# Kernel tuning notes

Measured on AMD Instinct MI355X. Metric: run time of the kernel, lower is better.

Reference implementation:

```python
import jax, jax.numpy as jnp
import numpy as np

EPS = 1e-5

def conv2d(x, w, b=None, pad=1):
    y = jax.lax.conv_general_dilated(x, w, (1, 1), [(pad, pad), (pad, pad)],
                                     dimension_numbers=('NCHW', 'OIHW', 'NCHW'))
    if b is not None:
        y = y + b[None, :, None, None]
    return y

def batchnorm(x, g, b):
    m = x.mean((0, 2, 3), keepdims=True)
    v = x.var((0, 2, 3), keepdims=True)
    return g[None, :, None, None] * (x - m) * jax.lax.rsqrt(v + EPS) + b[None, :, None, None]

def local_conv(x, w12):
    # x: [B,Ci,H,W]; w12: [B,Ci*9,H,W] -> per-pixel depthwise 3x3 conv
    B, Ci, H, W = x.shape
    xp = jnp.pad(x, ((0, 0), (0, 0), (1, 1), (1, 1)))
    patches = jnp.stack([xp[:, :, dh:dh + H, dw:dw + W]
                         for dh in range(3) for dw in range(3)], axis=2)  # [B,Ci,9,H,W]
    return (patches * w12.reshape(B, Ci, 9, H, W)).sum(axis=2)

def setup_inputs() -> dict:
    key = jax.random.key(0)
    ks = jax.random.split(key, 20)
    B, Ci, Cw, H, W = 4, 64, 64, 128, 128
    s = 0.05
    return {
        'input': jax.random.normal(ks[0], (B, Ci, H, W), jnp.float32),
        'weight': jax.random.normal(ks[1], (B, Cw, H, W), jnp.float32),
        'w_conv11': jax.random.normal(ks[2], (Ci, Ci + Cw, 3, 3), jnp.float32) * s,
        'b_conv11': jnp.zeros((Ci,), jnp.float32),
        'w_conv12': jax.random.normal(ks[3], (Ci * 9, Ci, 3, 3), jnp.float32) * s,
        'b_conv12': jnp.zeros((Ci * 9,), jnp.float32),
        'w_conv21': jax.random.normal(ks[4], (Ci, Ci + Cw, 3, 3), jnp.float32) * s,
        'b_conv21': jnp.zeros((Ci,), jnp.float32),
        'w_conv22': jax.random.normal(ks[5], (Ci * Ci, Ci, 1, 1), jnp.float32) * s,
        'b_conv22': jnp.zeros((Ci * Ci,), jnp.float32),
        'local_bn_g': jnp.ones((Ci,), jnp.float32),
        'local_bn_b': jnp.zeros((Ci,), jnp.float32),
        'br_g': jnp.ones((Ci,), jnp.float32),
        'br_b': jnp.zeros((Ci,), jnp.float32),
        'w_conv3': jax.random.normal(ks[6], (Ci, Ci, 3, 3), jnp.float32) * s,
        'conv3_bn_g': jnp.ones((Ci,), jnp.float32),
        'conv3_bn_b': jnp.zeros((Ci,), jnp.float32),
    }

def reference(input, weight, w_conv11, b_conv11, w_conv12, b_conv12,
              w_conv21, b_conv21, w_conv22, b_conv22,
              local_bn_g, local_bn_b, br_g, br_b,
              w_conv3, conv3_bn_g, conv3_bn_b):
    B, Ci, H, W = input.shape
    cat = jnp.concatenate([input, weight], axis=1)
    w11 = jax.nn.relu(conv2d(cat, w_conv11, b_conv11))
    w12 = conv2d(w11, w_conv12, b_conv12)                      # [B,Ci*9,H,W]
    w21 = jax.nn.relu(conv2d(cat, w_conv21, b_conv21))
    pooled = w21.mean((2, 3), keepdims=True)                   # [B,Ci,1,1]
    w22 = conv2d(pooled, w_conv22, b_conv22, pad=0).reshape(B, Ci, Ci)
    out1 = jax.nn.relu(batchnorm(local_conv(input, w12), local_bn_g, local_bn_b))
    out2 = jnp.einsum('bij,bjn->bin', w22, out1.reshape(B, Ci, H * W)).reshape(B, Ci, H, W)
    out3 = jax.nn.relu(batchnorm(out2, br_g, br_b))
    out4 = jax.nn.relu(batchnorm(conv2d(out3, w_conv3, None), conv3_bn_g, conv3_bn_b))
    return out4
```

## Files before the change

kernel.cpp:

```cpp
#include <hip/hip_runtime.h>

#define EPSV 1e-5f
#define HP 130
#define HW 16384

typedef unsigned int u32;
typedef unsigned short bfu;
typedef __bf16 bf16x8 __attribute__((ext_vector_type(8)));
typedef float  f32x4  __attribute__((ext_vector_type(4)));

__device__ __forceinline__ bfu f2bf(float f){
  u32 u = __builtin_bit_cast(u32, f);
  return (bfu)((u + 0x7FFFu + ((u >> 16) & 1u)) >> 16);
}
__device__ __forceinline__ float bf2f(bfu h){
  return __builtin_bit_cast(float, ((u32)h) << 16);
}
__device__ __forceinline__ f32x4 mfma16(bf16x8 a, bf16x8 b, f32x4 c){
  return __builtin_amdgcn_mfma_f32_16x16x32_bf16(a, b, c, 0, 0, 0);
}
__device__ __forceinline__ bf16x8 ldsfrag(const bfu* p){
  return __builtin_bit_cast(bf16x8, *(const uint4*)p);
}
__device__ __forceinline__ void gload_lds16(const uint4* g, uint4* l){
  __builtin_amdgcn_global_load_lds(
      (const __attribute__((address_space(1))) unsigned int*)g,
      (__attribute__((address_space(3))) unsigned int*)l, 16, 0, 0);
}


__global__ void k_zero_border(bfu* catT, bfu* w11T, bfu* out3T){
  int i = blockIdx.x*256 + threadIdx.x;
  if (i >= 4*516) return;
  int b = i/516, r = i - b*516;
  int hp, wpp;
  if (r < 130){ hp = 0; wpp = r; }
  else if (r < 260){ hp = 129; wpp = r - 130; }
  else { int r2 = r - 260; hp = 1 + (r2 >> 1); wpp = (r2 & 1)*129; }
  int pix = (b*HP + hp)*HP + wpp;
  uint4 z = {0,0,0,0};
  uint4* c4 = (uint4*)catT  + (size_t)pix*16;
  uint4* w4 = (uint4*)w11T  + (size_t)pix*8;
  uint4* o4 = (uint4*)out3T + (size_t)pix*8;
  #pragma unroll
  for (int k = 0; k < 16; ++k) c4[k] = z;
  #pragma unroll
  for (int k = 0; k < 8; ++k){ w4[k] = z; o4[k] = z; }
}

__global__ void k_prep_w(const float* __restrict__ w11w, const float* __restrict__ w21w,
                         const float* __restrict__ w12w, const float* __restrict__ w3w,
                         bfu* A11, bfu* A12, bfu* A3){
  const int total = 147456 + 331776 + 36864;
  for (int i = blockIdx.x*256 + threadIdx.x; i < total; i += gridDim.x*256){
    float v; bfu* dst;
    if (i < 147456){
      int tap = i >> 14, och = (i >> 7) & 127, cin = i & 127;
      v = (och < 64) ? w11w[(och*128 + cin)*9 + tap] : w21w[((och-64)*128 + cin)*9 + tap];
      dst = A11 + i;
    } else if (i < 147456 + 331776){
      int i2 = i - 147456;
      int g = i2 >> 12, t = g/9, tap2 = g%9;
      int c = (i2 >> 6) & 63, j = i2 & 63;
      v = w12w[((c*9 + t)*64 + j)*9 + tap2];
      dst = A12 + i2;
    } else {
      int i3 = i - (147456 + 331776);
      int tap2 = i3 >> 12, oc = (i3 >> 6) & 63, j = i3 & 63;
      v = w3w[(oc*64 + j)*9 + tap2];
      dst = A3 + i3;
    }
    *dst = f2bf(v);
  }
}

__global__ void k_prep_cat(const float* __restrict__ inp, const float* __restrict__ wgt, bfu* catT){
  __shared__ bfu lds[128*136];
  int b = blockIdx.y, h = blockIdx.x;
  int t = threadIdx.x;
  int w = t & 127, c0 = t >> 7;
  #pragma unroll 1
  for (int c = c0; c < 128; c += 2){
    const float* src = (c < 64) ? inp + ((b*64 + c)*128 + h)*128
                                : wgt + ((b*64 + (c-64))*128 + h)*128;
    lds[w*136 + c] = f2bf(src[w]);
  }
  __syncthreads();
  uint4* dst = (uint4*)catT;
  #pragma unroll
  for (int k = 0; k < 8; ++k){
    int idx = k*256 + t;
    int pix = idx >> 4, sub = idx & 15;
    uint4 v = *(const uint4*)&lds[pix*136 + sub*8];
    dst[(((b*HP + h+1)*HP) + (pix+1))*16 + sub] = v;
  }
}

__global__ __launch_bounds__(256) void k1_conv(
    const bfu* __restrict__ catT, const bfu* __restrict__ A11,
    const float* __restrict__ b11, const float* __restrict__ b21,
    bfu* __restrict__ w11T, float* __restrict__ poolP){
  __shared__ bfu ldsC[180*128];
  __shared__ bfu ldsA[2*8192];
  __shared__ float statsF[128];
  int tid = threadIdx.x;
  int b = blockIdx.y, tile = blockIdx.x;
  int h0 = (tile >> 3)*8, w0 = (tile & 7)*16;

  int wid = tid >> 6, l = tid & 63, lg = l >> 4, pc = l & 15;
  int wm = wid >> 1, wn = wid & 1;
  int pcT = tid & 15, lgT = (tid >> 4) & 3;

  const uint4* A4 = (const uint4*)A11;
  uint4* ldsA4 = (uint4*)ldsA;

  #pragma unroll
  for (int k = 0; k < 4; ++k){
    int q = k*4 + wid;
    int row = (q >> 1)*16 + pcT;
    gload_lds16(A4 + row*16 + (q&1)*4 + lgT, ldsA4 + k*256 + wid*64);
  }

  const uint4* catT4 = (const uint4*)catT;
  for (int s = tid; s < 180*16; s += 256){
    int cell = s >> 4, sub = s & 15;
    int th = cell/18, tw = cell - th*18;
    uint4 v = catT4[(((b*HP + h0+th)*HP) + (w0+tw))*16 + sub];
    *(uint4*)&ldsC[cell*128 + ((sub*8) ^ ((cell&7)<<3))] = v;
  }
  __syncthreads();

  f32x4 acc[4][4];
  #pragma unroll
  for (int i = 0; i < 4; ++i)
    #pragma unroll
    for (int j = 0; j < 4; ++j) acc[i][j] = f32x4{0.f,0.f,0.f,0.f};

  int cur = 0;
  #pragma unroll 1
  for (int cc = 0; cc < 18; ++cc){
    int tap = cc >> 1, p = cc & 1;
    if (cc < 17){
      int cc1 = cc + 1, tap1 = cc1 >> 1, p1 = cc1 & 1;
      #pragma unroll
      for (int k = 0; k < 4; ++k){
        int q = k*4 + wid;
        int row = (q >> 1)*16 + pcT;
        gload_lds16(A4 + tap1*2048 + row*16 + p1*8 + (q&1)*4 + lgT,
                    ldsA4 + (cur^1)*1024 + k*256 + wid*64);
      }
    }
    int kh = (tap >= 6) ? 2 : ((tap >= 3) ? 1 : 0);
    int kw = tap - kh*3;
    #pragma unroll
    for (int jq = 0; jq < 2; ++jq){
      int jc = p*2 + jq;
      bf16x8 a[4], bb[4];
      #pragma unroll
      for (int fm = 0; fm < 4; ++fm)
        a[fm] = __builtin_bit_cast(bf16x8, ldsA4[cur*1024 + ((wm*4 + fm)*2 + jq)*64 + l]);
      #pragma unroll
      for (int fn = 0; fn < 4; ++fn){
        int cell = (wn*4 + fn + kh)*18 + (pc + kw);
        bb[fn] = ldsfrag(&ldsC[cell*128 + ((jc*32 + lg*8) ^ ((cell&7)<<3))]);
      }
      #pragma unroll
      for (int fm = 0; fm < 4; ++fm)
        #pragma unroll
        for (int fn = 0; fn < 4; ++fn)
          acc[fm][fn] = mfma16(a[fm], bb[fn], acc[fm][fn]);
    }
    __syncthreads();
    cur ^= 1;
  }

  if (wm == 0){
    #pragma unroll
    for (int fm = 0; fm < 4; ++fm)
      #pragma unroll
      for (int r = 0; r < 4; ++r){
        int och = fm*16 + lg*4 + r;
        float bias = b11[och];
        #pragma unroll
        for (int fn = 0; fn < 4; ++fn){
          float v = acc[fm][fn][r] + bias;
          v = v > 0.f ? v : 0.f;
          int px = wn*64 + fn*16 + pc;
          ldsC[px*72 + och] = f2bf(v);
        }
      }
  } else {
    #pragma unroll
    for (int fm = 0; fm < 4; ++fm)
      #pragma unroll
      for (int r = 0; r < 4; ++r){
        int cw = fm*16 + lg*4 + r;
        float bias = b21[cw];
        float s = 0.f;
        #pragma unroll
        for (int fn = 0; fn < 4; ++fn){
          float v = acc[fm][fn][r] + bias;
          s += (v > 0.f ? v : 0.f);
        }
        s += __shfl_xor(s,1); s += __shfl_xor(s,2); s += __shfl_xor(s,4); s += __shfl_xor(s,8);
        if (pc == 0) statsF[wn*64 + cw] = s;
      }
  }
  __syncthreads();

  if (wid < 2){
    int px = tid;
    int h = h0 + (px >> 4), w = w0 + (px & 15);
    uint4* dst = (uint4*)w11T + (((b*HP + h+1)*HP) + (w+1))*8;
    const uint4* srcT = (const uint4*)&ldsC[px*72];
    #pragma unroll
    for (int k = 0; k < 8; ++k) dst[k] = srcT[k];
  }
  if (tid < 64)
    poolP[(b*128 + tile)*64 + tid] = statsF[tid] + statsF[64 + tid];
}

__global__ void k2a_pool(const float* __restrict__ poolP, float* pooled){
  int t = threadIdx.x;
  int b = t >> 6, c = t & 63;
  float s = 0.f;
  for (int tile = 0; tile < 128; ++tile) s += poolP[(b*128 + tile)*64 + c];
  pooled[t] = s * (1.f/16384.f);
}

__global__ void k2b_w22(const float* __restrict__ pooled, const float* __restrict__ W22,
                        const float* __restrict__ b22, bfu* __restrict__ w22bf){
  __shared__ float pl[64];
  int b = blockIdx.x >> 4, og = blockIdx.x & 15;
  if (threadIdx.x < 64) pl[threadIdx.x] = pooled[b*64 + threadIdx.x];
  __syncthreads();
  int o = og*256 + threadIdx.x;
  float acc = b22[o];
  #pragma unroll 4
  for (int c = 0; c < 64; ++c) acc += pl[c]*W22[o*64 + c];
  w22bf[b*4096 + o] = f2bf(acc);
}

__global__ __launch_bounds__(256) void k3_fused(
    const bfu* __restrict__ w11T, const bfu* __restrict__ catT,
    const bfu* __restrict__ A12, const float* __restrict__ b12,
    float* __restrict__ out1, float* __restrict__ st1){
  __shared__ bfu ldsW[180*64];
  __shared__ bfu ldsA[2*1536*8];
  __shared__ float b12f[576];
  __shared__ float wp[512];
  int tid = threadIdx.x;
  int b = blockIdx.y, tile = blockIdx.x;
  int h0 = (tile >> 3)*8, w0 = (tile & 7)*16;

  int wid = tid >> 6, l = tid & 63, lg = l >> 4, pc = l & 15;
  int w2 = wid*2;

  const uint4* A4 = (const uint4*)A12;
  uint4* ldsA4 = (uint4*)ldsA;
  int srcA = ((tid >> 7)*16 + (tid & 15))*8 + ((tid >> 6) & 1)*4 + ((tid >> 4) & 3);
  uint4* dstBase = ldsA4 + wid*64;

  {
    const uint4* sb = A4 + srcA;
    #pragma unroll
    for (int q = 0; q < 6; ++q)
      gload_lds16(sb + (q>>1)*512 + ((q&1)<<8), dstBase + (q>>1)*512 + ((q&1)<<8));
  }

  const uint4* w11T4 = (const uint4*)w11T;
  for (int s = tid; s < 180*8; s += 256){
    int cell = s >> 3, sub = s & 7;
    int th = cell/18, tw = cell - th*18;
    uint4 v = w11T4[(((b*HP + h0+th)*HP) + (w0+tw))*8 + sub];
    *(uint4*)&ldsW[cell*64 + ((sub*8) ^ ((cell&7)<<3))] = v;
  }
  for (int i = tid; i < 576; i += 256) b12f[i] = b12[i];
  __syncthreads();

  f32x4 oacc[4][2];
  #pragma unroll
  for (int i = 0; i < 4; ++i){ oacc[i][0] = f32x4{0.f,0.f,0.f,0.f}; oacc[i][1] = f32x4{0.f,0.f,0.f,0.f}; }
  f32x4 y[4][2];
  int cur = 0;

  #pragma unroll 1
  for (int cc = 0; cc < 27; ++cc){
    int tt = cc/3, m3 = cc - tt*3;
    if (cc < 26){
      const uint4* sb = A4 + (size_t)((cc+1)*3)*512 + srcA;
      uint4* db = dstBase + (cur^1)*1536;
      #pragma unroll
      for (int q = 0; q < 6; ++q)
        gload_lds16(sb + (q>>1)*512 + ((q&1)<<8), db + (q>>1)*512 + ((q&1)<<8));
    }
    if (m3 == 0){
      #pragma unroll
      for (int i = 0; i < 4; ++i){ y[i][0] = f32x4{0.f,0.f,0.f,0.f}; y[i][1] = f32x4{0.f,0.f,0.f,0.f}; }
    }
    #pragma unroll
    for (int t3 = 0; t3 < 3; ++t3){
      #pragma unroll
      for (int jc = 0; jc < 2; ++jc){
        bf16x8 a[4], bbf[2];
        #pragma unroll
        for (int fm = 0; fm < 4; ++fm)
          a[fm] = __builtin_bit_cast(bf16x8, ldsA4[cur*1536 + t3*512 + (fm*2 + jc)*64 + l]);
        #pragma unroll
        for (int fn = 0; fn < 2; ++fn){
          int cell = (w2 + fn + m3)*18 + (pc + t3);
          bbf[fn] = ldsfrag(&ldsW[cell*64 + ((jc*32 + lg*8) ^ ((cell&7)<<3))]);
        }
        #pragma unroll
        for (int fm = 0; fm < 4; ++fm)
          #pragma unroll
          for (int fn = 0; fn < 2; ++fn)
            y[fm][fn] = mfma16(a[fm], bbf[fn], y[fm][fn]);
      }
    }
    __syncthreads();
    if (m3 == 2){
      int dh = tt/3, dw = tt - dh*3;
      #pragma unroll
      for (int fn = 0; fn < 2; ++fn){
        const bfu* base = catT + ((size_t)((b*HP + h0 + w2 + fn + dh)*HP) + (w0 + pc + dw))*128 + lg*4;
        #pragma unroll
        for (int fm = 0; fm < 4; ++fm){
          ushort4 iv = *(const ushort4*)(base + fm*16);
          float i0 = bf2f(iv.x), i1 = bf2f(iv.y), i2 = bf2f(iv.z), i3 = bf2f(iv.w);
          int c = fm*16 + lg*4;
          oacc[fm][fn][0] += i0 * (y[fm][fn][0] + b12f[(c+0)*9 + tt]);
          oacc[fm][fn][1] += i1 * (y[fm][fn][1] + b12f[(c+1)*9 + tt]);
          oacc[fm][fn][2] += i2 * (y[fm][fn][2] + b12f[(c+2)*9 + tt]);
          oacc[fm][fn][3] += i3 * (y[fm][fn][3] + b12f[(c+3)*9 + tt]);
        }
      }
    }
    cur ^= 1;
  }

  #pragma unroll
  for (int fm = 0; fm < 4; ++fm)
    #pragma unroll
    for (int r = 0; r < 4; ++r){
      int c = fm*16 + lg*4 + r;
      float s = 0.f, ss = 0.f;
      #pragma unroll
      for (int fn = 0; fn < 2; ++fn){
        float v = oacc[fm][fn][r];
        out1[((b*64 + c)*128 + h0 + w2 + fn)*128 + (w0 + pc)] = v;
        s += v; ss += v*v;
      }
      s += __shfl_xor(s,1); s += __shfl_xor(s,2); s += __shfl_xor(s,4); s += __shfl_xor(s,8);
      ss += __shfl_xor(ss,1); ss += __shfl_xor(ss,2); ss += __shfl_xor(ss,4); ss += __shfl_xor(ss,8);
      if (pc == 0){ wp[(wid*64 + c)*2] = s; wp[(wid*64 + c)*2 + 1] = ss; }
    }
  __syncthreads();
  if (tid < 64){
    float s = 0.f, ss = 0.f;
    #pragma unroll
    for (int w = 0; w < 4; ++w){ s += wp[(w*64 + tid)*2]; ss += wp[(w*64 + tid)*2 + 1]; }
    int blin = b*128 + tile;
    st1[(blin*64 + tid)*2] = s; st1[(blin*64 + tid)*2 + 1] = ss;
  }
}

__global__ void k_bnstat(const float* __restrict__ st, int nblk, float n,
                         const float* __restrict__ g, const float* __restrict__ bb, float* bn){
  __shared__ float red[512];
  int tid = threadIdx.x;
  int c = tid & 63, kk = tid >> 6;
  float s = 0.f, ss = 0.f;
  for (int k = kk; k < nblk; k += 4){
    float2 v = *(const float2*)&st[(k*64 + c)*2];
    s += v.x; ss += v.y;
  }
  red[tid*2] = s; red[tid*2 + 1] = ss;
  __syncthreads();
  if (tid < 64){
    #pragma unroll
    for (int q = 1; q < 4; ++q){ s += red[(q*64 + tid)*2]; ss += red[(q*64 + tid)*2 + 1]; }
    float mean = s/n, var = ss/n - mean*mean;
    float a = g[tid]*rsqrtf(var + EPSV);
    bn[tid*2] = a; bn[tid*2 + 1] = bb[tid] - mean*a;
  }
}

__global__ __launch_bounds__(256) void k4_einsum(
    const float* __restrict__ out1, const bfu* __restrict__ w22bf,
    const float* __restrict__ bn1, float* __restrict__ out2, float* __restrict__ st2){
  __shared__ bfu ldsX[256*72];
  __shared__ float a1[64], be1[64];
  __shared__ float wp[512];
  int tid = threadIdx.x;
  int b = blockIdx.y, chunk = blockIdx.x;
  if (tid < 64){ a1[tid] = bn1[tid*2]; be1[tid] = bn1[tid*2 + 1]; }
  __syncthreads();
  int p0 = chunk*256;

  {
    int px = tid;
    const float* src = out1 + (size_t)(b*64)*HW + p0 + px;
    #pragma unroll 1
    for (int j0 = 0; j0 < 64; j0 += 4){
      float x0 = src[(j0+0)*HW]; x0 = a1[j0+0]*x0 + be1[j0+0]; x0 = x0 > 0.f ? x0 : 0.f;
      float x1 = src[(j0+1)*HW]; x1 = a1[j0+1]*x1 + be1[j0+1]; x1 = x1 > 0.f ? x1 : 0.f;
      float x2 = src[(j0+2)*HW]; x2 = a1[j0+2]*x2 + be1[j0+2]; x2 = x2 > 0.f ? x2 : 0.f;
      float x3 = src[(j0+3)*HW]; x3 = a1[j0+3]*x3 + be1[j0+3]; x3 = x3 > 0.f ? x3 : 0.f;
      ushort4 pk; pk.x = f2bf(x0); pk.y = f2bf(x1); pk.z = f2bf(x2); pk.w = f2bf(x3);
      *(ushort4*)&ldsX[px*72 + j0] = pk;
    }
  }
  __syncthreads();

  int wid = tid >> 6, l = tid & 63, lg = l >> 4, pc = l & 15;
  const uint4* W4 = (const uint4*)w22bf;
  f32x4 acc[4][4];
  #pragma unroll
  for (int i = 0; i < 4; ++i)
    #pragma unroll
    for (int j = 0; j < 4; ++j) acc[i][j] = f32x4{0.f,0.f,0.f,0.f};

  #pragma unroll
  for (int jc = 0; jc < 2; ++jc){
    bf16x8 a[4], bb[4];
    #pragma unroll
    for (int fm = 0; fm < 4; ++fm)
      a[fm] = __builtin_bit_cast(bf16x8, W4[b*512 + (fm*16 + pc)*8 + jc*4 + lg]);
    #pragma unroll
    for (int fn = 0; fn < 4; ++fn)
      bb[fn] = ldsfrag(&ldsX[(wid*64 + fn*16 + pc)*72 + jc*32 + lg*8]);
    #pragma unroll
    for (int fm = 0; fm < 4; ++fm)
      #pragma unroll
      for (int fn = 0; fn < 4; ++fn)
        acc[fm][fn] = mfma16(a[fm], bb[fn], acc[fm][fn]);
  }

  #pragma unroll
  for (int fm = 0; fm < 4; ++fm)
    #pragma unroll
    for (int r = 0; r < 4; ++r){
      int i = fm*16 + lg*4 + r;
      float s = 0.f, ss = 0.f;
      #pragma unroll
      for (int fn = 0; fn < 4; ++fn){
        int px = wid*64 + fn*16 + pc;
        float v = acc[fm][fn][r];
        out2[(b*64 + i)*HW + p0 + px] = v;
        s += v; ss += v*v;
      }
      s += __shfl_xor(s,1); s += __shfl_xor(s,2); s += __shfl_xor(s,4); s += __shfl_xor(s,8);
      ss += __shfl_xor(ss,1); ss += __shfl_xor(ss,2); ss += __shfl_xor(ss,4); ss += __shfl_xor(ss,8);
      if (pc == 0){ wp[(wid*64 + i)*2] = s; wp[(wid*64 + i)*2 + 1] = ss; }
    }
  __syncthreads();
  if (tid < 64){
    float s = 0.f, ss = 0.f;
    #pragma unroll
    for (int w = 0; w < 4; ++w){ s += wp[(w*64 + tid)*2]; ss += wp[(w*64 + tid)*2 + 1]; }
    int blin = b*64 + chunk;
    st2[(blin*64 + tid)*2] = s; st2[(blin*64 + tid)*2 + 1] = ss;
  }
}

__global__ void k4c_out3(const float* __restrict__ out2, const float* __restrict__ bn2, bfu* out3T){
  __shared__ bfu lds[128*72];
  int b = blockIdx.y, h = blockIdx.x;
  int t = threadIdx.x;
  int px = t & 127, ch = (t >> 7)*32;
  #pragma unroll 1
  for (int cc = 0; cc < 32; cc += 4){
    int c = ch + cc;
    float x0 = out2[((b*64 + c+0) << 14) + (h << 7) + px];
    float x1 = out2[((b*64 + c+1) << 14) + (h << 7) + px];
    float x2 = out2[((b*64 + c+2) << 14) + (h << 7) + px];
    float x3 = out2[((b*64 + c+3) << 14) + (h << 7) + px];
    x0 = bn2[(c+0)*2]*x0 + bn2[(c+0)*2+1]; x0 = x0 > 0.f ? x0 : 0.f;
    x1 = bn2[(c+1)*2]*x1 + bn2[(c+1)*2+1]; x1 = x1 > 0.f ? x1 : 0.f;
    x2 = bn2[(c+2)*2]*x2 + bn2[(c+2)*2+1]; x2 = x2 > 0.f ? x2 : 0.f;
    x3 = bn2[(c+3)*2]*x3 + bn2[(c+3)*2+1]; x3 = x3 > 0.f ? x3 : 0.f;
    ushort4 pk; pk.x = f2bf(x0); pk.y = f2bf(x1); pk.z = f2bf(x2); pk.w = f2bf(x3);
    *(ushort4*)&lds[px*72 + c] = pk;
  }
  __syncthreads();
  uint4* dst = (uint4*)out3T;
  #pragma unroll
  for (int k = 0; k < 4; ++k){
    int idx = k*256 + t;
    int pix = idx >> 3, sub = idx & 7;
    uint4 v = *(const uint4*)&lds[pix*72 + sub*8];
    dst[((size_t)(b*HP + h+1)*HP + (pix+1))*8 + sub] = v;
  }
}

__global__ __launch_bounds__(256) void k5_conv3(
    const bfu* __restrict__ out3T, const bfu* __restrict__ A3,
    float* __restrict__ outc, float* __restrict__ st3){
  __shared__ bfu lds[180*72];
  __shared__ float wp[512];
  int tid = threadIdx.x;
  int b = blockIdx.y, tile = blockIdx.x;
  int h0 = (tile >> 3)*8, w0 = (tile & 7)*16;
  const uint4* src4 = (const uint4*)out3T;
  for (int s = tid; s < 180*8; s += 256){
    int cell = s >> 3, sub = s & 7;
    int th = cell/18, tw = cell - th*18;
    *(uint4*)&lds[cell*72 + sub*8] = src4[(((b*HP + h0+th)*HP) + (w0+tw))*8 + sub];
  }
  __syncthreads();

  int wid = tid >> 6, l = tid & 63, lg = l >> 4, pc = l & 15;
  f32x4 acc[4][2];
  #pragma unroll
  for (int i = 0; i < 4; ++i){ acc[i][0] = f32x4{0.f,0.f,0.f,0.f}; acc[i][1] = f32x4{0.f,0.f,0.f,0.f}; }
  const uint4* A4 = (const uint4*)A3;
  #pragma unroll 3
  for (int tap2 = 0; tap2 < 9; ++tap2){
    int kh = tap2/3, kw = tap2 - kh*3;
    #pragma unroll
    for (int jc = 0; jc < 2; ++jc){
      bf16x8 a[4], bb[2];
      #pragma unroll
      for (int fm = 0; fm < 4; ++fm)
        a[fm] = __builtin_bit_cast(bf16x8, A4[tap2*512 + (fm*16 + pc)*8 + jc*4 + lg]);
      #pragma unroll
      for (int fn = 0; fn < 2; ++fn){
        int cell = (wid*2 + fn + kh)*18 + (pc + kw);
        bb[fn] = ldsfrag(&lds[cell*72 + jc*32 + lg*8]);
      }
      #pragma unroll
      for (int fm = 0; fm < 4; ++fm)
        #pragma unroll
        for (int fn = 0; fn < 2; ++fn)
          acc[fm][fn] = mfma16(a[fm], bb[fn], acc[fm][fn]);
    }
  }
  #pragma unroll
  for (int fm = 0; fm < 4; ++fm)
    #pragma unroll
    for (int r = 0; r < 4; ++r){
      int c = fm*16 + lg*4 + r;
      float s = 0.f, ss = 0.f;
      #pragma unroll
      for (int fn = 0; fn < 2; ++fn){
        int pr = wid*2 + fn;
        float v = acc[fm][fn][r];
        outc[((b*64 + c)*128 + h0 + pr)*128 + (w0 + pc)] = v;
        s += v; ss += v*v;
      }
      s += __shfl_xor(s,1); s += __shfl_xor(s,2); s += __shfl_xor(s,4); s += __shfl_xor(s,8);
      ss += __shfl_xor(ss,1); ss += __shfl_xor(ss,2); ss += __shfl_xor(ss,4); ss += __shfl_xor(ss,8);
      if (pc == 0){ wp[(wid*64 + c)*2] = s; wp[(wid*64 + c)*2 + 1] = ss; }
    }
  __syncthreads();
  if (tid < 64){
    float s = 0.f, ss = 0.f;
    #pragma unroll
    for (int w = 0; w < 4; ++w){ s += wp[(w*64 + tid)*2]; ss += wp[(w*64 + tid)*2 + 1]; }
    int blin = b*128 + tile;
    st3[(blin*64 + tid)*2] = s; st3[(blin*64 + tid)*2 + 1] = ss;
  }
}

__global__ void k6_final(float4* __restrict__ out, const float* __restrict__ bn3){
  const int total4 = 4*64*HW/4;
  for (int i = blockIdx.x*256 + threadIdx.x; i < total4; i += gridDim.x*256){
    int c = (i >> 12) & 63;
    float a = bn3[c*2], be = bn3[c*2 + 1];
    float4 x = out[i];
    x.x = a*x.x + be; x.x = x.x > 0.f ? x.x : 0.f;
    x.y = a*x.y + be; x.y = x.y > 0.f ? x.y : 0.f;
    x.z = a*x.z + be; x.z = x.z > 0.f ? x.z : 0.f;
    x.w = a*x.w + be; x.w = x.w > 0.f ? x.w : 0.f;
    out[i] = x;
  }
}

extern "C" void kernel_launch(void* const* d_in, const int* in_sizes, int n_in,
                              void* d_out, int out_size, void* d_ws, size_t ws_size,
                              hipStream_t stream){
  const float* inp  = (const float*)d_in[0];
  const float* wgt  = (const float*)d_in[1];
  const float* w11w = (const float*)d_in[2];
  const float* b11  = (const float*)d_in[3];
  const float* w12w = (const float*)d_in[4];
  const float* b12  = (const float*)d_in[5];
  const float* w21w = (const float*)d_in[6];
  const float* b21  = (const float*)d_in[7];
  const float* W22  = (const float*)d_in[8];
  const float* b22  = (const float*)d_in[9];
  const float* lg   = (const float*)d_in[10];
  const float* lb   = (const float*)d_in[11];
  const float* brg  = (const float*)d_in[12];
  const float* brb  = (const float*)d_in[13];
  const float* w3w  = (const float*)d_in[14];
  const float* c3g  = (const float*)d_in[15];
  const float* c3b  = (const float*)d_in[16];

  if (ws_size < 53200000) return;

  char* ws = (char*)d_ws;
  bfu*   catT  = (bfu*)(ws);
  bfu*   w11T  = (bfu*)(ws + 17305600);
  bfu*   out3T = (bfu*)(ws + 25958400);
  bfu*   A11   = (bfu*)(ws + 34611200);
  bfu*   A12   = (bfu*)(ws + 34906112);
  bfu*   A3    = (bfu*)(ws + 35569664);
  float* out1  = (float*)(ws + 35643392);
  float* poolP = (float*)(ws + 52420608);
  float* pooled= (float*)(ws + 52551680);
  bfu*   w22bf = (bfu*)(ws + 52552704);
  float* st13  = (float*)(ws + 52585472);
  float* bn1   = (float*)(ws + 52847616);
  float* st2   = (float*)(ws + 52848128);
  float* bn2   = (float*)(ws + 52979200);
  float* bn3   = (float*)(ws + 52979712);
  float* outF  = (float*)d_out;

  k_zero_border<<<dim3(9),  dim3(256), 0, stream>>>(catT, w11T, out3T);
  k_prep_w  <<<dim3(512),  dim3(256), 0, stream>>>(w11w, w21w, w12w, w3w, A11, A12, A3);
  k_prep_cat<<<dim3(128,4),dim3(256), 0, stream>>>(inp, wgt, catT);
  k1_conv   <<<dim3(128,4),dim3(256), 0, stream>>>(catT, A11, b11, b21, w11T, poolP);
  k2a_pool  <<<dim3(1),    dim3(256), 0, stream>>>(poolP, pooled);
  k2b_w22   <<<dim3(64),   dim3(256), 0, stream>>>(pooled, W22, b22, w22bf);
  k3_fused  <<<dim3(128,4),dim3(256), 0, stream>>>(w11T, catT, A12, b12, out1, st13);
  k_bnstat  <<<dim3(1),    dim3(256), 0, stream>>>(st13, 512, 65536.f, lg, lb, bn1);
  k4_einsum <<<dim3(64,4), dim3(256), 0, stream>>>(out1, w22bf, bn1, outF, st2);
  k_bnstat  <<<dim3(1),    dim3(256), 0, stream>>>(st2, 256, 65536.f, brg, brb, bn2);
  k4c_out3  <<<dim3(128,4),dim3(256), 0, stream>>>(outF, bn2, out3T);
  k5_conv3  <<<dim3(128,4),dim3(256), 0, stream>>>(out3T, A3, outF, st13);
  k_bnstat  <<<dim3(1),    dim3(256), 0, stream>>>(st13, 512, 65536.f, c3g, c3b, bn3);
  k6_final  <<<dim3(1024), dim3(256), 0, stream>>>((float4*)outF, bn3);
}
```

Measured before the change: 275.3 us.

## Merge prep kernels and fold BN-stat reductions into consumer kernels

Collapses the border-zeroing, weight-prep and input-transpose kernels into one launch. The pooling reduction moves into the w22 kernel, and each single-block BN statistics kernel is removed by recomputing the per-channel scale and shift redundantly in every block of the consuming kernel. This cuts the launch count from 14 to 8 and removes serialized one-block kernels. In exchange, every consumer block re-reads the partial statistics (up to 512x64 float2) before doing its real work, and the final kernel now uses fewer blocks.

Result: no change. 278.7 us (+1.2%).

```diff
diff --git a/kernel.cpp b/kernel.cpp
--- a/kernel.cpp
+++ b/kernel.cpp
@@ -28,31 +28,56 @@
       (__attribute__((address_space(3))) unsigned int*)l, 16, 0, 0);
 }
 
-
-__global__ void k_zero_border(bfu* catT, bfu* w11T, bfu* out3T){
-  int i = blockIdx.x*256 + threadIdx.x;
-  if (i >= 4*516) return;
-  int b = i/516, r = i - b*516;
-  int hp, wpp;
-  if (r < 130){ hp = 0; wpp = r; }
-  else if (r < 260){ hp = 129; wpp = r - 130; }
-  else { int r2 = r - 260; hp = 1 + (r2 >> 1); wpp = (r2 & 1)*129; }
-  int pix = (b*HP + hp)*HP + wpp;
-  uint4 z = {0,0,0,0};
-  uint4* c4 = (uint4*)catT  + (size_t)pix*16;
-  uint4* w4 = (uint4*)w11T  + (size_t)pix*8;
-  uint4* o4 = (uint4*)out3T + (size_t)pix*8;
-  #pragma unroll
-  for (int k = 0; k < 16; ++k) c4[k] = z;
-  #pragma unroll
-  for (int k = 0; k < 8; ++k){ w4[k] = z; o4[k] = z; }
-}
-
-__global__ void k_prep_w(const float* __restrict__ w11w, const float* __restrict__ w21w,
-                         const float* __restrict__ w12w, const float* __restrict__ w3w,
-                         bfu* A11, bfu* A12, bfu* A3){
+__global__ __launch_bounds__(256) void k_prep(
+    const float* __restrict__ inp, const float* __restrict__ wgt,
+    const float* __restrict__ w11w, const float* __restrict__ w21w,
+    const float* __restrict__ w12w, const float* __restrict__ w3w,
+    bfu* catT, bfu* A11, bfu* A12, bfu* A3, bfu* w11T, bfu* out3T){
+  __shared__ bfu lds[128*136];
+  int bx = blockIdx.x, by = blockIdx.y;
+  int t = threadIdx.x;
+
+  if (bx < 128){
+    int b = by, h = bx;
+    int w = t & 127, c0 = t >> 7;
+    #pragma unroll 1
+    for (int c = c0; c < 128; c += 2){
+      const float* src = (c < 64) ? inp + ((b*64 + c)*128 + h)*128
+                                  : wgt + ((b*64 + (c-64))*128 + h)*128;
+      lds[w*136 + c] = f2bf(src[w]);
+    }
+    __syncthreads();
+    uint4* dst = (uint4*)catT;
+    #pragma unroll
+    for (int k = 0; k < 8; ++k){
+      int idx = k*256 + t;
+      int pix = idx >> 4, sub = idx & 15;
+      uint4 v = *(const uint4*)&lds[pix*136 + sub*8];
+      dst[(((b*HP + h+1)*HP) + (pix+1))*16 + sub] = v;
+    }
+    return;
+  }
+
+  int r = (bx - 128)*4 + by;
+  const int STR = 24*256;
+  for (int i = r*256 + t; i < 4*516; i += STR){
+    int b = i/516, rr = i - b*516;
+    int hp, wpp;
+    if (rr < 130){ hp = 0; wpp = rr; }
+    else if (rr < 260){ hp = 129; wpp = rr - 130; }
+    else { int r2 = rr - 260; hp = 1 + (r2 >> 1); wpp = (r2 & 1)*129; }
+    int pix = (b*HP + hp)*HP + wpp;
+    uint4 z = {0,0,0,0};
+    uint4* c4 = (uint4*)catT  + (size_t)pix*16;
+    uint4* w4 = (uint4*)w11T  + (size_t)pix*8;
+    uint4* o4 = (uint4*)out3T + (size_t)pix*8;
+    #pragma unroll
+    for (int k = 0; k < 16; ++k) c4[k] = z;
+    #pragma unroll
+    for (int k = 0; k < 8; ++k){ w4[k] = z; o4[k] = z; }
+  }
   const int total = 147456 + 331776 + 36864;
-  for (int i = blockIdx.x*256 + threadIdx.x; i < total; i += gridDim.x*256){
+  for (int i = r*256 + t; i < total; i += STR){
     float v; bfu* dst;
     if (i < 147456){
       int tap = i >> 14, och = (i >> 7) & 127, cin = i & 127;
@@ -60,9 +85,9 @@
       dst = A11 + i;
     } else if (i < 147456 + 331776){
       int i2 = i - 147456;
-      int g = i2 >> 12, t = g/9, tap2 = g%9;
+      int g = i2 >> 12, tt = g/9, tap2 = g%9;
       int c = (i2 >> 6) & 63, j = i2 & 63;
-      v = w12w[((c*9 + t)*64 + j)*9 + tap2];
+      v = w12w[((c*9 + tt)*64 + j)*9 + tap2];
       dst = A12 + i2;
     } else {
       int i3 = i - (147456 + 331776);
@@ -71,28 +96,6 @@
       dst = A3 + i3;
     }
     *dst = f2bf(v);
-  }
-}
-
-__global__ void k_prep_cat(const float* __restrict__ inp, const float* __restrict__ wgt, bfu* catT){
-  __shared__ bfu lds[128*136];
-  int b = blockIdx.y, h = blockIdx.x;
-  int t = threadIdx.x;
-  int w = t & 127, c0 = t >> 7;
-  #pragma unroll 1
-  for (int c = c0; c < 128; c += 2){
-    const float* src = (c < 64) ? inp + ((b*64 + c)*128 + h)*128
-                                : wgt + ((b*64 + (c-64))*128 + h)*128;
-    lds[w*136 + c] = f2bf(src[w]);
-  }
-  __syncthreads();
-  uint4* dst = (uint4*)catT;
-  #pragma unroll
-  for (int k = 0; k < 8; ++k){
-    int idx = k*256 + t;
-    int pix = idx >> 4, sub = idx & 15;
-    uint4 v = *(const uint4*)&lds[pix*136 + sub*8];
-    dst[(((b*HP + h+1)*HP) + (pix+1))*16 + sub] = v;
   }
 }
 
@@ -220,21 +223,19 @@
     poolP[(b*128 + tile)*64 + tid] = statsF[tid] + statsF[64 + tid];
 }
 
-__global__ void k2a_pool(const float* __restrict__ poolP, float* pooled){
-  int t = threadIdx.x;
-  int b = t >> 6, c = t & 63;
-  float s = 0.f;
-  for (int tile = 0; tile < 128; ++tile) s += poolP[(b*128 + tile)*64 + c];
-  pooled[t] = s * (1.f/16384.f);
-}
-
-__global__ void k2b_w22(const float* __restrict__ pooled, const float* __restrict__ W22,
-                        const float* __restrict__ b22, bfu* __restrict__ w22bf){
+__global__ __launch_bounds__(256) void k2_w22(
+    const float* __restrict__ poolP, const float* __restrict__ W22,
+    const float* __restrict__ b22, bfu* __restrict__ w22bf){
   __shared__ float pl[64];
   int b = blockIdx.x >> 4, og = blockIdx.x & 15;
-  if (threadIdx.x < 64) pl[threadIdx.x] = pooled[b*64 + threadIdx.x];
-  __syncthreads();
-  int o = og*256 + threadIdx.x;
+  int t = threadIdx.x;
+  if (t < 64){
+    float s = 0.f;
+    for (int tile = 0; tile < 128; ++tile) s += poolP[(b*128 + tile)*64 + t];
+    pl[t] = s * (1.f/16384.f);
+  }
+  __syncthreads();
+  int o = og*256 + t;
   float acc = b22[o];
   #pragma unroll 4
   for (int c = 0; c < 64; ++c) acc += pl[c]*W22[o*64 + c];
@@ -365,37 +366,34 @@
   }
 }
 
-__global__ void k_bnstat(const float* __restrict__ st, int nblk, float n,
-                         const float* __restrict__ g, const float* __restrict__ bb, float* bn){
-  __shared__ float red[512];
-  int tid = threadIdx.x;
-  int c = tid & 63, kk = tid >> 6;
-  float s = 0.f, ss = 0.f;
-  for (int k = kk; k < nblk; k += 4){
-    float2 v = *(const float2*)&st[(k*64 + c)*2];
-    s += v.x; ss += v.y;
-  }
-  red[tid*2] = s; red[tid*2 + 1] = ss;
-  __syncthreads();
-  if (tid < 64){
-    #pragma unroll
-    for (int q = 1; q < 4; ++q){ s += red[(q*64 + tid)*2]; ss += red[(q*64 + tid)*2 + 1]; }
-    float mean = s/n, var = ss/n - mean*mean;
-    float a = g[tid]*rsqrtf(var + EPSV);
-    bn[tid*2] = a; bn[tid*2 + 1] = bb[tid] - mean*a;
-  }
-}
-
 __global__ __launch_bounds__(256) void k4_einsum(
     const float* __restrict__ out1, const bfu* __restrict__ w22bf,
-    const float* __restrict__ bn1, float* __restrict__ out2, float* __restrict__ st2){
+    const float* __restrict__ st1, const float* __restrict__ lgm,
+    const float* __restrict__ lbt, float* __restrict__ out2, float* __restrict__ st2){
   __shared__ bfu ldsX[256*72];
   __shared__ float a1[64], be1[64];
   __shared__ float wp[512];
   int tid = threadIdx.x;
   int b = blockIdx.y, chunk = blockIdx.x;
-  if (tid < 64){ a1[tid] = bn1[tid*2]; be1[tid] = bn1[tid*2 + 1]; }
-  __syncthreads();
+
+  {
+    int c = tid & 63, kk = tid >> 6;
+    float s = 0.f, ss = 0.f;
+    for (int k = kk; k < 512; k += 4){
+      float2 v = *(const float2*)&st1[(k*64 + c)*2];
+      s += v.x; ss += v.y;
+    }
+    wp[tid*2] = s; wp[tid*2 + 1] = ss;
+    __syncthreads();
+    if (tid < 64){
+      #pragma unroll
+      for (int q = 1; q < 4; ++q){ s += wp[(q*64 + tid)*2]; ss += wp[(q*64 + tid)*2 + 1]; }
+      float mean = s/65536.f, var = ss/65536.f - mean*mean;
+      float a = lgm[tid]*rsqrtf(var + EPSV);
+      a1[tid] = a; be1[tid] = lbt[tid] - mean*a;
+    }
+    __syncthreads();
+  }
   int p0 = chunk*256;
 
   {
@@ -464,10 +462,34 @@
   }
 }
 
-__global__ void k4c_out3(const float* __restrict__ out2, const float* __restrict__ bn2, bfu* out3T){
+__global__ __launch_bounds__(256) void k4c_out3(
+    const float* __restrict__ out2, const float* __restrict__ st2,
+    const float* __restrict__ brg, const float* __restrict__ brb, bfu* out3T){
   __shared__ bfu lds[128*72];
+  __shared__ float red[512];
+  __shared__ float sa[64], sb[64];
   int b = blockIdx.y, h = blockIdx.x;
   int t = threadIdx.x;
+
+  {
+    int c = t & 63, kk = t >> 6;
+    float s = 0.f, ss = 0.f;
+    for (int k = kk; k < 256; k += 4){
+      float2 v = *(const float2*)&st2[(k*64 + c)*2];
+      s += v.x; ss += v.y;
+    }
+    red[t*2] = s; red[t*2 + 1] = ss;
+    __syncthreads();
+    if (t < 64){
+      #pragma unroll
+      for (int q = 1; q < 4; ++q){ s += red[(q*64 + t)*2]; ss += red[(q*64 + t)*2 + 1]; }
+      float mean = s/65536.f, var = ss/65536.f - mean*mean;
+      float a = brg[t]*rsqrtf(var + EPSV);
+      sa[t] = a; sb[t] = brb[t] - mean*a;
+    }
+    __syncthreads();
+  }
+
   int px = t & 127, ch = (t >> 7)*32;
   #pragma unroll 1
   for (int cc = 0; cc < 32; cc += 4){
@@ -476,10 +498,10 @@
     float x1 = out2[((b*64 + c+1) << 14) + (h << 7) + px];
     float x2 = out2[((b*64 + c+2) << 14) + (h << 7) + px];
     float x3 = out2[((b*64 + c+3) << 14) + (h << 7) + px];
-    x0 = bn2[(c+0)*2]*x0 + bn2[(c+0)*2+1]; x0 = x0 > 0.f ? x0 : 0.f;
-    x1 = bn2[(c+1)*2]*x1 + bn2[(c+1)*2+1]; x1 = x1 > 0.f ? x1 : 0.f;
-    x2 = bn2[(c+2)*2]*x2 + bn2[(c+2)*2+1]; x2 = x2 > 0.f ? x2 : 0.f;
-    x3 = bn2[(c+3)*2]*x3 + bn2[(c+3)*2+1]; x3 = x3 > 0.f ? x3 : 0.f;
+    x0 = sa[c+0]*x0 + sb[c+0]; x0 = x0 > 0.f ? x0 : 0.f;
+    x1 = sa[c+1]*x1 + sb[c+1]; x1 = x1 > 0.f ? x1 : 0.f;
+    x2 = sa[c+2]*x2 + sb[c+2]; x2 = x2 > 0.f ? x2 : 0.f;
+    x3 = sa[c+3]*x3 + sb[c+3]; x3 = x3 > 0.f ? x3 : 0.f;
     ushort4 pk; pk.x = f2bf(x0); pk.y = f2bf(x1); pk.z = f2bf(x2); pk.w = f2bf(x3);
     *(ushort4*)&lds[px*72 + c] = pk;
   }
@@ -563,11 +585,34 @@
   }
 }
 
-__global__ void k6_final(float4* __restrict__ out, const float* __restrict__ bn3){
+__global__ __launch_bounds__(256) void k6_final(
+    float4* __restrict__ out, const float* __restrict__ st3,
+    const float* __restrict__ c3g, const float* __restrict__ c3b){
+  __shared__ float red[512];
+  __shared__ float sa[64], sb[64];
+  int tid = threadIdx.x;
+  {
+    int c = tid & 63, kk = tid >> 6;
+    float s = 0.f, ss = 0.f;
+    for (int k = kk; k < 512; k += 4){
+      float2 v = *(const float2*)&st3[(k*64 + c)*2];
+      s += v.x; ss += v.y;
+    }
+    red[tid*2] = s; red[tid*2 + 1] = ss;
+    __syncthreads();
+    if (tid < 64){
+      #pragma unroll
+      for (int q = 1; q < 4; ++q){ s += red[(q*64 + tid)*2]; ss += red[(q*64 + tid)*2 + 1]; }
+      float mean = s/65536.f, var = ss/65536.f - mean*mean;
+      float a = c3g[tid]*rsqrtf(var + EPSV);
+      sa[tid] = a; sb[tid] = c3b[tid] - mean*a;
+    }
+    __syncthreads();
+  }
   const int total4 = 4*64*HW/4;
-  for (int i = blockIdx.x*256 + threadIdx.x; i < total4; i += gridDim.x*256){
+  for (int i = blockIdx.x*256 + tid; i < total4; i += 256*256){
     int c = (i >> 12) & 63;
-    float a = bn3[c*2], be = bn3[c*2 + 1];
+    float a = sa[c], be = sb[c];
     float4 x = out[i];
     x.x = a*x.x + be; x.x = x.x > 0.f ? x.x : 0.f;
     x.y = a*x.y + be; x.y = x.y > 0.f ? x.y : 0.f;
@@ -609,27 +654,18 @@
   bfu*   A3    = (bfu*)(ws + 35569664);
   float* out1  = (float*)(ws + 35643392);
   float* poolP = (float*)(ws + 52420608);
-  float* pooled= (float*)(ws + 52551680);
   bfu*   w22bf = (bfu*)(ws + 52552704);
   float* st13  = (float*)(ws + 52585472);
-  float* bn1   = (float*)(ws + 52847616);
   float* st2   = (float*)(ws + 52848128);
-  float* bn2   = (float*)(ws + 52979200);
-  float* bn3   = (float*)(ws + 52979712);
   float* outF  = (float*)d_out;
 
-  k_zero_border<<<dim3(9),  dim3(256), 0, stream>>>(catT, w11T, out3T);
-  k_prep_w  <<<dim3(512),  dim3(256), 0, stream>>>(w11w, w21w, w12w, w3w, A11, A12, A3);
-  k_prep_cat<<<dim3(128,4),dim3(256), 0, stream>>>(inp, wgt, catT);
-  k1_conv   <<<dim3(128,4),dim3(256), 0, stream>>>(catT, A11, b11, b21, w11T, poolP);
-  k2a_pool  <<<dim3(1),    dim3(256), 0, stream>>>(poolP, pooled);
-  k2b_w22   <<<dim3(64),   dim3(256), 0, stream>>>(pooled, W22, b22, w22bf);
-  k3_fused  <<<dim3(128,4),dim3(256), 0, stream>>>(w11T, catT, A12, b12, out1, st13);
-  k_bnstat  <<<dim3(1),    dim3(256), 0, stream>>>(st13, 512, 65536.f, lg, lb, bn1);
-  k4_einsum <<<dim3(64,4), dim3(256), 0, stream>>>(out1, w22bf, bn1, outF, st2);
-  k_bnstat  <<<dim3(1),    dim3(256), 0, stream>>>(st2, 256, 65536.f, brg, brb, bn2);
-  k4c_out3  <<<dim3(128,4),dim3(256), 0, stream>>>(outF, bn2, out3T);
-  k5_conv3  <<<dim3(128,4),dim3(256), 0, stream>>>(out3T, A3, outF, st13);
-  k_bnstat  <<<dim3(1),    dim3(256), 0, stream>>>(st13, 512, 65536.f, c3g, c3b, bn3);
-  k6_final  <<<dim3(1024), dim3(256), 0, stream>>>((float4*)outF, bn3);
-}
+  k_prep   <<<dim3(134,4), dim3(256), 0, stream>>>(inp, wgt, w11w, w21w, w12w, w3w,
+                                                   catT, A11, A12, A3, w11T, out3T);
+  k1_conv  <<<dim3(128,4), dim3(256), 0, stream>>>(catT, A11, b11, b21, w11T, poolP);
+  k2_w22   <<<dim3(64),    dim3(256), 0, stream>>>(poolP, W22, b22, w22bf);
+  k3_fused <<<dim3(128,4), dim3(256), 0, stream>>>(w11T, catT, A12, b12, out1, st13);
+  k4_einsum<<<dim3(64,4),  dim3(256), 0, stream>>>(out1, w22bf, st13, lg, lb, outF, st2);
+  k4c_out3 <<<dim3(128,4), dim3(256), 0, stream>>>(outF, st2, brg, brb, out3T);
+  k5_conv3 <<<dim3(128,4), dim3(256), 0, stream>>>(out3T, A3, outF, st13);
+  k6_final <<<dim3(256),   dim3(256), 0, stream>>>((float4*)outF, st13, c3g, c3b);
+}
```
